# Kernel optimization log

Hardware: AMD Instinct MI355X
Metric: run time of the kernel (lower is better)

The kernel has to match this reference:

```python
import jax, jax.numpy as jnp
import numpy as np

N_NODES = 50000


def setup_inputs() -> dict:
    key = jax.random.key(0)
    ks = jax.random.split(key, 6)
    L, d = 3, 128
    x = jax.random.normal(ks[0], (N_NODES, d), dtype=jnp.float32)
    edge_index = jax.random.randint(ks[1], (2, 640000), 0, N_NODES, dtype=jnp.int64)
    s = 1.0 / np.sqrt(d)
    W1 = jax.random.normal(ks[2], (L, d, d), dtype=jnp.float32) * s
    W2 = jax.random.normal(ks[3], (L, d, d), dtype=jnp.float32) * s
    b1 = jnp.zeros((L, d), dtype=jnp.float32)
    b2 = jnp.zeros((L, d), dtype=jnp.float32)
    eps = jnp.zeros((L,), dtype=jnp.float32)
    final_w = jax.random.normal(ks[4], (d + L * d, d), dtype=jnp.float32) / np.sqrt(d + L * d)
    final_b = jnp.zeros((d,), dtype=jnp.float32)
    return {"x": x, "edge_index": edge_index, "W1": W1, "b1": b1,
            "W2": W2, "b2": b2, "eps": eps, "final_w": final_w, "final_b": final_b}


def reference(x, edge_index, W1, b1, W2, b2, eps, final_w, final_b):
    src, dst = edge_index[0], edge_index[1]
    num_layers = W1.shape[0]
    xs = [x]
    h = x
    for l in range(num_layers):
        # GINConv: sum-aggregate neighbor features, add (1+eps)*self, then 2-layer MLP
        agg = jax.ops.segment_sum(h[src], dst, num_segments=N_NODES)  # [N, d]
        z = (1.0 + eps[l]) * h + agg
        z = jax.nn.relu(z @ W1[l] + b1[l])
        h = jax.nn.relu(z @ W2[l] + b2[l])
        xs.append(h)
    out = jnp.concatenate(xs, axis=-1)  # [N, in + L*out]
    return out @ final_w + final_b
```

## Files before the change

### kernel.cpp

```cpp
#include <hip/hip_runtime.h>

#define NNODES 50000
#define NEDGES 640000
#define D 128

typedef unsigned short u16;
typedef unsigned int u32;
typedef __bf16 bf16x8 __attribute__((ext_vector_type(8)));
typedef float f32x4 __attribute__((ext_vector_type(4)));
union AB { uint4 u4; bf16x8 f; };

__device__ __forceinline__ u16 f2b(float f) {
    u32 u = __float_as_uint(f);
    return (u16)((u + 0x7fffu + ((u >> 16) & 1u)) >> 16);
}
__device__ __forceinline__ u32 pack2(float lo, float hi) {
    return (u32)f2b(lo) | ((u32)f2b(hi) << 16);
}
__device__ __forceinline__ float blo(u32 v) { return __uint_as_float(v << 16); }
__device__ __forceinline__ float bhi(u32 v) { return __uint_as_float(v & 0xffff0000u); }


__global__ void k_hist(const int* __restrict__ dst, int* __restrict__ cnt) {
    int e = blockIdx.x * 256 + threadIdx.x;
    if (e < NEDGES) atomicAdd(&cnt[dst[e]], 1);
}

__global__ void k_scan1(const int* __restrict__ cnt, int* __restrict__ rp,
                        int* __restrict__ bsum) {
    __shared__ int s[256];
    int tid = threadIdx.x;
    int i = blockIdx.x * 256 + tid;
    int v = (i < NNODES) ? cnt[i] : 0;
    s[tid] = v;
    __syncthreads();
    for (int off = 1; off < 256; off <<= 1) {
        int t = (tid >= off) ? s[tid - off] : 0;
        __syncthreads();
        s[tid] += t;
        __syncthreads();
    }
    if (i < NNODES) rp[i] = s[tid] - v;
    if (tid == 255) bsum[blockIdx.x] = s[255];
}

__global__ void k_scan2(int* __restrict__ bsum, int nb) {
    __shared__ int s[256];
    int tid = threadIdx.x;
    int v = (tid < nb) ? bsum[tid] : 0;
    s[tid] = v;
    __syncthreads();
    for (int off = 1; off < 256; off <<= 1) {
        int t = (tid >= off) ? s[tid - off] : 0;
        __syncthreads();
        s[tid] += t;
        __syncthreads();
    }
    if (tid < nb) bsum[tid] = s[tid] - v;
}

__global__ void k_add(int* __restrict__ rp, const int* __restrict__ bsum) {
    int i = blockIdx.x * 256 + threadIdx.x;
    if (i < NNODES) rp[i] += bsum[blockIdx.x];
    if (i == 0) rp[NNODES] = NEDGES;
}

__global__ void k_scatter(const int* __restrict__ src, const int* __restrict__ dst,
                          const int* __restrict__ rp, int* __restrict__ fill,
                          int* __restrict__ srcs) {
    int e = blockIdx.x * 256 + threadIdx.x;
    if (e < NEDGES) {
        int dn = dst[e];
        int p = rp[dn] + atomicAdd(&fill[dn], 1);
        srcs[p] = src[e];
    }
}

__global__ void k_prep(const float* __restrict__ W1, const float* __restrict__ W2,
                       const float* __restrict__ fw, u16* __restrict__ wT1,
                       u16* __restrict__ wT2, u16* __restrict__ fwTc) {
    int idx = blockIdx.x * 256 + threadIdx.x;
    if (idx < 3 * 16384) {
        int l = idx >> 14, r = idx & 16383, n = r >> 7, k = r & 127;
        wT1[idx] = f2b(W1[l * 16384 + k * 128 + n]);
        wT2[idx] = f2b(W2[l * 16384 + k * 128 + n]);
    }
    if (idx < 4 * 16384) {
        int ch = idx >> 14, r = idx & 16383, n = r >> 7, k = r & 127;
        fwTc[idx] = f2b(fw[(ch * 128 + k) * 128 + n]);
    }
}

__global__ void k_cvt(const float* __restrict__ x, u32* __restrict__ xb) {
    int i = blockIdx.x * 256 + threadIdx.x;
    if (i < NNODES * 64) {
        float2 v = ((const float2*)x)[i];
        xb[i] = pack2(v.x, v.y);
    }
}

__global__ void k_agg(const uint4* __restrict__ h4, const int* __restrict__ rp,
                      const int* __restrict__ srcs, const float* __restrict__ epsp,
                      uint4* __restrict__ z4) {
    int tid = threadIdx.x;
    int c = tid & 15;
    int node = (blockIdx.x * 256 + tid) >> 4;
    int gbase = tid & 48;
    float sc = 1.0f + epsp[0];

    uint4 sv = h4[node * 16 + c];
    float acc[8];
    acc[0] = sc * blo(sv.x); acc[1] = sc * bhi(sv.x);
    acc[2] = sc * blo(sv.y); acc[3] = sc * bhi(sv.y);
    acc[4] = sc * blo(sv.z); acc[5] = sc * bhi(sv.z);
    acc[6] = sc * blo(sv.w); acc[7] = sc * bhi(sv.w);

    int beg = rp[node], end = rp[node + 1];
    for (int base = beg; base < end; base += 16) {
        int n = end - base; if (n > 16) n = 16;
        int myidx = (base + c < end) ? srcs[base + c] : 0;
        int j = 0;
        for (; j + 4 <= n; j += 4) {
            int s0 = __shfl(myidx, gbase + j + 0, 64);
            int s1 = __shfl(myidx, gbase + j + 1, 64);
            int s2 = __shfl(myidx, gbase + j + 2, 64);
            int s3 = __shfl(myidx, gbase + j + 3, 64);
            uint4 v0 = h4[s0 * 16 + c];
            uint4 v1 = h4[s1 * 16 + c];
            uint4 v2 = h4[s2 * 16 + c];
            uint4 v3 = h4[s3 * 16 + c];
            acc[0] += blo(v0.x) + blo(v1.x) + blo(v2.x) + blo(v3.x);
            acc[1] += bhi(v0.x) + bhi(v1.x) + bhi(v2.x) + bhi(v3.x);
            acc[2] += blo(v0.y) + blo(v1.y) + blo(v2.y) + blo(v3.y);
            acc[3] += bhi(v0.y) + bhi(v1.y) + bhi(v2.y) + bhi(v3.y);
            acc[4] += blo(v0.z) + blo(v1.z) + blo(v2.z) + blo(v3.z);
            acc[5] += bhi(v0.z) + bhi(v1.z) + bhi(v2.z) + bhi(v3.z);
            acc[6] += blo(v0.w) + blo(v1.w) + blo(v2.w) + blo(v3.w);
            acc[7] += bhi(v0.w) + bhi(v1.w) + bhi(v2.w) + bhi(v3.w);
        }
        for (; j < n; ++j) {
            int s0 = __shfl(myidx, gbase + j, 64);
            uint4 v0 = h4[s0 * 16 + c];
            acc[0] += blo(v0.x); acc[1] += bhi(v0.x);
            acc[2] += blo(v0.y); acc[3] += bhi(v0.y);
            acc[4] += blo(v0.z); acc[5] += bhi(v0.z);
            acc[6] += blo(v0.w); acc[7] += bhi(v0.w);
        }
    }

    uint4 o;
    o.x = pack2(acc[0], acc[1]);
    o.y = pack2(acc[2], acc[3]);
    o.z = pack2(acc[4], acc[5]);
    o.w = pack2(acc[6], acc[7]);
    z4[node * 16 + c] = o;
}

__launch_bounds__(256, 2)
__global__ void k_mlp(const u16* __restrict__ A, const u16* __restrict__ wT1g,
                      const float* __restrict__ b1, const u16* __restrict__ wT2g,
                      const float* __restrict__ b2, u16* __restrict__ H) {
    __shared__ u16 wbuf[128 * 128];
    __shared__ u16 Tb[128 * 128];
    int tid = threadIdx.x;
    int wave = tid >> 6, lane = tid & 63, l16 = lane & 15, quad = lane >> 4;
    int r0 = blockIdx.x * 128 + wave * 32;

    {
        const uint4* g = (const uint4*)wT1g;
        for (int i = tid; i < 2048; i += 256) ((uint4*)wbuf)[i] = g[i];
    }

    AB a[2][4];
#pragma unroll
    for (int s = 0; s < 2; ++s) {
        int row = r0 + s * 16 + l16;
#pragma unroll
        for (int kb = 0; kb < 4; ++kb) {
            if (row < NNODES)
                a[s][kb].u4 = *(const uint4*)&A[row * 128 + kb * 32 + quad * 8];
            else
                a[s][kb].u4 = make_uint4(0, 0, 0, 0);
        }
    }
    __syncthreads();

    f32x4 acc[2][8];
#pragma unroll
    for (int col = 0; col < 8; ++col) {
        float bv = b1[col * 16 + l16];
        acc[0][col] = (f32x4){bv, bv, bv, bv};
        acc[1][col] = (f32x4){bv, bv, bv, bv};
    }
#pragma unroll
    for (int col = 0; col < 8; ++col) {
#pragma unroll
        for (int kb = 0; kb < 4; ++kb) {
            AB b;
            b.u4 = *(const uint4*)&wbuf[(col * 16 + l16) * 128 + kb * 32 + quad * 8];
            acc[0][col] = __builtin_amdgcn_mfma_f32_16x16x32_bf16(a[0][kb].f, b.f, acc[0][col], 0, 0, 0);
            acc[1][col] = __builtin_amdgcn_mfma_f32_16x16x32_bf16(a[1][kb].f, b.f, acc[1][col], 0, 0, 0);
        }
    }

#pragma unroll
    for (int s = 0; s < 2; ++s)
#pragma unroll
        for (int col = 0; col < 8; ++col)
#pragma unroll
            for (int r = 0; r < 4; ++r) {
                float v = fmaxf(acc[s][col][r], 0.f);
                Tb[(wave * 32 + s * 16 + quad * 4 + r) * 128 + col * 16 + l16] = f2b(v);
            }
    __syncthreads();

    {
        const uint4* g = (const uint4*)wT2g;
        for (int i = tid; i < 2048; i += 256) ((uint4*)wbuf)[i] = g[i];
    }
    AB a2[2][4];
#pragma unroll
    for (int s = 0; s < 2; ++s)
#pragma unroll
        for (int kb = 0; kb < 4; ++kb)
            a2[s][kb].u4 = *(const uint4*)&Tb[(wave * 32 + s * 16 + l16) * 128 + kb * 32 + quad * 8];
    __syncthreads();

#pragma unroll
    for (int col = 0; col < 8; ++col) {
        float bv = b2[col * 16 + l16];
        acc[0][col] = (f32x4){bv, bv, bv, bv};
        acc[1][col] = (f32x4){bv, bv, bv, bv};
    }
#pragma unroll
    for (int col = 0; col < 8; ++col) {
#pragma unroll
        for (int kb = 0; kb < 4; ++kb) {
            AB b;
            b.u4 = *(const uint4*)&wbuf[(col * 16 + l16) * 128 + kb * 32 + quad * 8];
            acc[0][col] = __builtin_amdgcn_mfma_f32_16x16x32_bf16(a2[0][kb].f, b.f, acc[0][col], 0, 0, 0);
            acc[1][col] = __builtin_amdgcn_mfma_f32_16x16x32_bf16(a2[1][kb].f, b.f, acc[1][col], 0, 0, 0);
        }
    }
#pragma unroll
    for (int s = 0; s < 2; ++s)
#pragma unroll
        for (int col = 0; col < 8; ++col)
#pragma unroll
            for (int r = 0; r < 4; ++r) {
                float v = fmaxf(acc[s][col][r], 0.f);
                Tb[(wave * 32 + s * 16 + quad * 4 + r) * 128 + col * 16 + l16] = f2b(v);
            }
    __syncthreads();

    for (int i = tid; i < 2048; i += 256) {
        int r = i >> 4, cc = i & 15;
        int grow = blockIdx.x * 128 + r;
        if (grow < NNODES)
            *(uint4*)&H[grow * 128 + cc * 8] = *(const uint4*)&Tb[r * 128 + cc * 8];
    }
}

__launch_bounds__(256, 2)
__global__ void k_final(const u16* __restrict__ xb, const u16* __restrict__ h1,
                        const u16* __restrict__ h2b, const u16* __restrict__ h3,
                        const u16* __restrict__ fwTc, const float* __restrict__ fb,
                        float* __restrict__ out) {
    __shared__ u16 wbuf[128 * 128];
    int tid = threadIdx.x;
    int wave = tid >> 6, lane = tid & 63, l16 = lane & 15, quad = lane >> 4;
    int r0 = blockIdx.x * 128 + wave * 32;

    f32x4 acc[2][8];
#pragma unroll
    for (int col = 0; col < 8; ++col) {
        float bv = fb[col * 16 + l16];
        acc[0][col] = (f32x4){bv, bv, bv, bv};
        acc[1][col] = (f32x4){bv, bv, bv, bv};
    }

    const u16* chin[4] = {xb, h1, h2b, h3};
    for (int ch = 0; ch < 4; ++ch) {
        __syncthreads();
        {
            const uint4* g = (const uint4*)(fwTc + ch * 16384);
            for (int i = tid; i < 2048; i += 256) ((uint4*)wbuf)[i] = g[i];
        }
        const u16* cp = chin[ch];
        AB a[2][4];
#pragma unroll
        for (int s = 0; s < 2; ++s) {
            int row = r0 + s * 16 + l16;
#pragma unroll
            for (int kb = 0; kb < 4; ++kb) {
                if (row < NNODES)
                    a[s][kb].u4 = *(const uint4*)&cp[row * 128 + kb * 32 + quad * 8];
                else
                    a[s][kb].u4 = make_uint4(0, 0, 0, 0);
            }
        }
        __syncthreads();
#pragma unroll
        for (int col = 0; col < 8; ++col) {
#pragma unroll
            for (int kb = 0; kb < 4; ++kb) {
                AB b;
                b.u4 = *(const uint4*)&wbuf[(col * 16 + l16) * 128 + kb * 32 + quad * 8];
                acc[0][col] = __builtin_amdgcn_mfma_f32_16x16x32_bf16(a[0][kb].f, b.f, acc[0][col], 0, 0, 0);
                acc[1][col] = __builtin_amdgcn_mfma_f32_16x16x32_bf16(a[1][kb].f, b.f, acc[1][col], 0, 0, 0);
            }
        }
    }

#pragma unroll
    for (int s = 0; s < 2; ++s)
#pragma unroll
        for (int col = 0; col < 8; ++col)
#pragma unroll
            for (int r = 0; r < 4; ++r) {
                int row = r0 + s * 16 + quad * 4 + r;
                if (row < NNODES) out[row * 128 + col * 16 + l16] = acc[s][col][r];
            }
}

extern "C" void kernel_launch(void* const* d_in, const int* in_sizes, int n_in,
                              void* d_out, int out_size, void* d_ws, size_t ws_size,
                              hipStream_t stream) {
    const float* x   = (const float*)d_in[0];
    const int*   ei  = (const int*)d_in[1];
    const float* W1  = (const float*)d_in[2];
    const float* b1  = (const float*)d_in[3];
    const float* W2  = (const float*)d_in[4];
    const float* b2  = (const float*)d_in[5];
    const float* eps = (const float*)d_in[6];
    const float* fw  = (const float*)d_in[7];
    const float* fb  = (const float*)d_in[8];
    float* out = (float*)d_out;

    const int* srcA = ei;
    const int* dstA = ei + NEDGES;

    char* p = (char*)d_ws;
    size_t off = 0;
    auto take = [&](size_t bytes) {
        char* r = p + off;
        off = (off + bytes + 255) & ~(size_t)255;
        return r;
    };
    int* rp   = (int*)take((NNODES + 1) * sizeof(int));
    int* cnt  = (int*)take(NNODES * sizeof(int));
    int* fill = (int*)take(NNODES * sizeof(int));
    int* bsum = (int*)take(256 * sizeof(int));
    int* srcs = (int*)take(NEDGES * sizeof(int));
    u16* wT1  = (u16*)take(3 * 16384 * sizeof(u16));
    u16* wT2  = (u16*)take(3 * 16384 * sizeof(u16));
    u16* fwTc = (u16*)take(4 * 16384 * sizeof(u16));
    u16* xb   = (u16*)take((size_t)NNODES * D * sizeof(u16));
    u16* zb   = (u16*)take((size_t)NNODES * D * sizeof(u16));
    u16* hb1  = (u16*)take((size_t)NNODES * D * sizeof(u16));
    u16* hb2  = (u16*)take((size_t)NNODES * D * sizeof(u16));
    u16* hb3  = (u16*)take((size_t)NNODES * D * sizeof(u16));
    (void)ws_size; (void)in_sizes; (void)n_in; (void)out_size;

    hipMemsetAsync(cnt, 0, NNODES * sizeof(int), stream);
    hipMemsetAsync(fill, 0, NNODES * sizeof(int), stream);

    k_prep<<<(4 * 16384 + 255) / 256, 256, 0, stream>>>(W1, W2, fw, wT1, wT2, fwTc);
    k_cvt<<<(NNODES * 64 + 255) / 256, 256, 0, stream>>>(x, (u32*)xb);

    int nb = (NNODES + 255) / 256;
    k_hist<<<(NEDGES + 255) / 256, 256, 0, stream>>>(dstA, cnt);
    k_scan1<<<nb, 256, 0, stream>>>(cnt, rp, bsum);
    k_scan2<<<1, 256, 0, stream>>>(bsum, nb);
    k_add<<<nb, 256, 0, stream>>>(rp, bsum);
    k_scatter<<<(NEDGES + 255) / 256, 256, 0, stream>>>(srcA, dstA, rp, fill, srcs);

    const u16* hin = xb;
    u16* houts[3] = {hb1, hb2, hb3};
    int gm = (NNODES + 127) / 128;
    for (int l = 0; l < 3; ++l) {
        k_agg<<<NNODES * 16 / 256, 256, 0, stream>>>((const uint4*)hin, rp, srcs, eps + l, (uint4*)zb);
        k_mlp<<<gm, 256, 0, stream>>>(zb, wT1 + l * 16384, b1 + l * D,
                                      wT2 + l * 16384, b2 + l * D, houts[l]);
        hin = houts[l];
    }
    k_final<<<gm, 256, 0, stream>>>(xb, hb1, hb2, hb3, fwTc, fb, out);
}
```

Measured before the change: 319.9 us.

## Fuse neighbor aggregation into MLP kernel with swizzled LDS and merged prep

Aggregation is now done inside the MLP kernel. Each block gathers and sums neighbor features for its 128 rows straight into shared memory, so the intermediate z buffer is no longer written to and read back from global memory, and three kernel launches are removed. Shared-memory tiles for weights and activations use an XOR-style chunk rotation to avoid bank conflicts, and the gather loop is unrolled to 8. The CSR scatter reuses the count array with atomicSub, which drops one memset, and the weight prep and x conversion are merged into one kernel. The risk is less parallelism in the gather: 391 blocks each walking 128 nodes serially, versus many small blocks before, which may leave memory latency less hidden.

```diff
diff --git a/kernel.cpp b/kernel.cpp
--- a/kernel.cpp
+++ b/kernel.cpp
@@ -19,6 +19,13 @@
 }
 __device__ __forceinline__ float blo(u32 v) { return __uint_as_float(v << 16); }
 __device__ __forceinline__ float bhi(u32 v) { return __uint_as_float(v & 0xffff0000u); }
+
+__device__ __forceinline__ void acc8(float* a, uint4 v) {
+    a[0] += blo(v.x); a[1] += bhi(v.x);
+    a[2] += blo(v.y); a[3] += bhi(v.y);
+    a[4] += blo(v.z); a[5] += bhi(v.z);
+    a[6] += blo(v.w); a[7] += bhi(v.w);
+}
 
 
 __global__ void k_hist(const int* __restrict__ dst, int* __restrict__ cnt) {
@@ -66,19 +73,20 @@
 }
 
 __global__ void k_scatter(const int* __restrict__ src, const int* __restrict__ dst,
-                          const int* __restrict__ rp, int* __restrict__ fill,
+                          const int* __restrict__ rp, int* __restrict__ cnt,
                           int* __restrict__ srcs) {
     int e = blockIdx.x * 256 + threadIdx.x;
     if (e < NEDGES) {
         int dn = dst[e];
-        int p = rp[dn] + atomicAdd(&fill[dn], 1);
-        srcs[p] = src[e];
+        int old = atomicSub(&cnt[dn], 1);
+        srcs[rp[dn] + old - 1] = src[e];
     }
 }
 
 __global__ void k_prep(const float* __restrict__ W1, const float* __restrict__ W2,
-                       const float* __restrict__ fw, u16* __restrict__ wT1,
-                       u16* __restrict__ wT2, u16* __restrict__ fwTc) {
+                       const float* __restrict__ fw, const float* __restrict__ x,
+                       u16* __restrict__ wT1, u16* __restrict__ wT2,
+                       u16* __restrict__ fwTc, u32* __restrict__ xb) {
     int idx = blockIdx.x * 256 + threadIdx.x;
     if (idx < 3 * 16384) {
         int l = idx >> 14, r = idx & 16383, n = r >> 7, k = r & 127;
@@ -89,101 +97,103 @@
         int ch = idx >> 14, r = idx & 16383, n = r >> 7, k = r & 127;
         fwTc[idx] = f2b(fw[(ch * 128 + k) * 128 + n]);
     }
-}
-
-__global__ void k_cvt(const float* __restrict__ x, u32* __restrict__ xb) {
-    int i = blockIdx.x * 256 + threadIdx.x;
-    if (i < NNODES * 64) {
-        float2 v = ((const float2*)x)[i];
-        xb[i] = pack2(v.x, v.y);
-    }
-}
-
-__global__ void k_agg(const uint4* __restrict__ h4, const int* __restrict__ rp,
+    if (idx < NNODES * 64) {
+        float2 v = ((const float2*)x)[idx];
+        xb[idx] = pack2(v.x, v.y);
+    }
+}
+
+__launch_bounds__(256, 2)
+__global__ void k_mlp(const uint4* __restrict__ h4, const int* __restrict__ rp,
                       const int* __restrict__ srcs, const float* __restrict__ epsp,
-                      uint4* __restrict__ z4) {
+                      const u16* __restrict__ wT1g, const float* __restrict__ b1,
+                      const u16* __restrict__ wT2g, const float* __restrict__ b2,
+                      u16* __restrict__ H) {
+    __shared__ u16 Tb[128 * 128];
+    __shared__ u16 wbuf[128 * 128];
+    uint4* Tb4 = (uint4*)Tb;
+    uint4* wb4 = (uint4*)wbuf;
     int tid = threadIdx.x;
-    int c = tid & 15;
-    int node = (blockIdx.x * 256 + tid) >> 4;
-    int gbase = tid & 48;
-    float sc = 1.0f + epsp[0];
-
-    uint4 sv = h4[node * 16 + c];
-    float acc[8];
-    acc[0] = sc * blo(sv.x); acc[1] = sc * bhi(sv.x);
-    acc[2] = sc * blo(sv.y); acc[3] = sc * bhi(sv.y);
-    acc[4] = sc * blo(sv.z); acc[5] = sc * bhi(sv.z);
-    acc[6] = sc * blo(sv.w); acc[7] = sc * bhi(sv.w);
-
-    int beg = rp[node], end = rp[node + 1];
-    for (int base = beg; base < end; base += 16) {
-        int n = end - base; if (n > 16) n = 16;
-        int myidx = (base + c < end) ? srcs[base + c] : 0;
-        int j = 0;
-        for (; j + 4 <= n; j += 4) {
-            int s0 = __shfl(myidx, gbase + j + 0, 64);
-            int s1 = __shfl(myidx, gbase + j + 1, 64);
-            int s2 = __shfl(myidx, gbase + j + 2, 64);
-            int s3 = __shfl(myidx, gbase + j + 3, 64);
-            uint4 v0 = h4[s0 * 16 + c];
-            uint4 v1 = h4[s1 * 16 + c];
-            uint4 v2 = h4[s2 * 16 + c];
-            uint4 v3 = h4[s3 * 16 + c];
-            acc[0] += blo(v0.x) + blo(v1.x) + blo(v2.x) + blo(v3.x);
-            acc[1] += bhi(v0.x) + bhi(v1.x) + bhi(v2.x) + bhi(v3.x);
-            acc[2] += blo(v0.y) + blo(v1.y) + blo(v2.y) + blo(v3.y);
-            acc[3] += bhi(v0.y) + bhi(v1.y) + bhi(v2.y) + bhi(v3.y);
-            acc[4] += blo(v0.z) + blo(v1.z) + blo(v2.z) + blo(v3.z);
-            acc[5] += bhi(v0.z) + bhi(v1.z) + bhi(v2.z) + bhi(v3.z);
-            acc[6] += blo(v0.w) + blo(v1.w) + blo(v2.w) + blo(v3.w);
-            acc[7] += bhi(v0.w) + bhi(v1.w) + bhi(v2.w) + bhi(v3.w);
-        }
-        for (; j < n; ++j) {
-            int s0 = __shfl(myidx, gbase + j, 64);
-            uint4 v0 = h4[s0 * 16 + c];
-            acc[0] += blo(v0.x); acc[1] += bhi(v0.x);
-            acc[2] += blo(v0.y); acc[3] += bhi(v0.y);
-            acc[4] += blo(v0.z); acc[5] += bhi(v0.z);
-            acc[6] += blo(v0.w); acc[7] += bhi(v0.w);
-        }
-    }
-
-    uint4 o;
-    o.x = pack2(acc[0], acc[1]);
-    o.y = pack2(acc[2], acc[3]);
-    o.z = pack2(acc[4], acc[5]);
-    o.w = pack2(acc[6], acc[7]);
-    z4[node * 16 + c] = o;
-}
-
-__launch_bounds__(256, 2)
-__global__ void k_mlp(const u16* __restrict__ A, const u16* __restrict__ wT1g,
-                      const float* __restrict__ b1, const u16* __restrict__ wT2g,
-                      const float* __restrict__ b2, u16* __restrict__ H) {
-    __shared__ u16 wbuf[128 * 128];
-    __shared__ u16 Tb[128 * 128];
-    int tid = threadIdx.x;
-    int wave = tid >> 6, lane = tid & 63, l16 = lane & 15, quad = lane >> 4;
-    int r0 = blockIdx.x * 128 + wave * 32;
+    int r0 = blockIdx.x * 128;
 
     {
         const uint4* g = (const uint4*)wT1g;
-        for (int i = tid; i < 2048; i += 256) ((uint4*)wbuf)[i] = g[i];
-    }
+        for (int i = tid; i < 2048; i += 256) {
+            int n = i >> 4, ch = i & 15;
+            wb4[n * 16 + ((ch + n) & 15)] = g[i];
+        }
+    }
+
+    {
+        int c = tid & 15;
+        int g16 = tid >> 4;
+        int gbase = tid & 48;
+        float sc = 1.0f + epsp[0];
+        for (int jn = 0; jn < 8; ++jn) {
+            int nl = g16 * 8 + jn;
+            int node = r0 + nl;
+            float acc[8] = {0.f, 0.f, 0.f, 0.f, 0.f, 0.f, 0.f, 0.f};
+            if (node < NNODES) {
+                uint4 sv = h4[node * 16 + c];
+                acc[0] = sc * blo(sv.x); acc[1] = sc * bhi(sv.x);
+                acc[2] = sc * blo(sv.y); acc[3] = sc * bhi(sv.y);
+                acc[4] = sc * blo(sv.z); acc[5] = sc * bhi(sv.z);
+                acc[6] = sc * blo(sv.w); acc[7] = sc * bhi(sv.w);
+                int beg = rp[node], end = rp[node + 1];
+                for (int base = beg; base < end; base += 16) {
+                    int n = end - base; if (n > 16) n = 16;
+                    int myidx = (base + c < end) ? srcs[base + c] : 0;
+                    int j = 0;
+                    for (; j + 8 <= n; j += 8) {
+                        int s0 = __shfl(myidx, gbase + j + 0, 64);
+                        int s1 = __shfl(myidx, gbase + j + 1, 64);
+                        int s2 = __shfl(myidx, gbase + j + 2, 64);
+                        int s3 = __shfl(myidx, gbase + j + 3, 64);
+                        int s4 = __shfl(myidx, gbase + j + 4, 64);
+                        int s5 = __shfl(myidx, gbase + j + 5, 64);
+                        int s6 = __shfl(myidx, gbase + j + 6, 64);
+                        int s7 = __shfl(myidx, gbase + j + 7, 64);
+                        uint4 v0 = h4[s0 * 16 + c]; uint4 v1 = h4[s1 * 16 + c];
+                        uint4 v2 = h4[s2 * 16 + c]; uint4 v3 = h4[s3 * 16 + c];
+                        uint4 v4 = h4[s4 * 16 + c]; uint4 v5 = h4[s5 * 16 + c];
+                        uint4 v6 = h4[s6 * 16 + c]; uint4 v7 = h4[s7 * 16 + c];
+                        acc8(acc, v0); acc8(acc, v1); acc8(acc, v2); acc8(acc, v3);
+                        acc8(acc, v4); acc8(acc, v5); acc8(acc, v6); acc8(acc, v7);
+                    }
+                    for (; j + 4 <= n; j += 4) {
+                        int s0 = __shfl(myidx, gbase + j + 0, 64);
+                        int s1 = __shfl(myidx, gbase + j + 1, 64);
+                        int s2 = __shfl(myidx, gbase + j + 2, 64);
+                        int s3 = __shfl(myidx, gbase + j + 3, 64);
+                        uint4 v0 = h4[s0 * 16 + c]; uint4 v1 = h4[s1 * 16 + c];
+                        uint4 v2 = h4[s2 * 16 + c]; uint4 v3 = h4[s3 * 16 + c];
+                        acc8(acc, v0); acc8(acc, v1); acc8(acc, v2); acc8(acc, v3);
+                    }
+                    for (; j < n; ++j) {
+                        int s0 = __shfl(myidx, gbase + j, 64);
+                        uint4 v0 = h4[s0 * 16 + c];
+                        acc8(acc, v0);
+                    }
+                }
+            }
+            uint4 o;
+            o.x = pack2(acc[0], acc[1]); o.y = pack2(acc[2], acc[3]);
+            o.z = pack2(acc[4], acc[5]); o.w = pack2(acc[6], acc[7]);
+            Tb4[nl * 16 + ((c + nl) & 15)] = o;
+        }
+    }
+    __syncthreads();
+
+    int wave = tid >> 6, lane = tid & 63, l16 = lane & 15, quad = lane >> 4;
 
     AB a[2][4];
 #pragma unroll
     for (int s = 0; s < 2; ++s) {
-        int row = r0 + s * 16 + l16;
-#pragma unroll
-        for (int kb = 0; kb < 4; ++kb) {
-            if (row < NNODES)
-                a[s][kb].u4 = *(const uint4*)&A[row * 128 + kb * 32 + quad * 8];
-            else
-                a[s][kb].u4 = make_uint4(0, 0, 0, 0);
-        }
-    }
-    __syncthreads();
+        int m = wave * 32 + s * 16 + l16;
+#pragma unroll
+        for (int kb = 0; kb < 4; ++kb)
+            a[s][kb].u4 = Tb4[m * 16 + ((kb * 4 + quad + m) & 15)];
+    }
 
     f32x4 acc[2][8];
 #pragma unroll
@@ -197,11 +207,13 @@
 #pragma unroll
         for (int kb = 0; kb < 4; ++kb) {
             AB b;
-            b.u4 = *(const uint4*)&wbuf[(col * 16 + l16) * 128 + kb * 32 + quad * 8];
+            int n = col * 16 + l16;
+            b.u4 = wb4[n * 16 + ((kb * 4 + quad + n) & 15)];
             acc[0][col] = __builtin_amdgcn_mfma_f32_16x16x32_bf16(a[0][kb].f, b.f, acc[0][col], 0, 0, 0);
             acc[1][col] = __builtin_amdgcn_mfma_f32_16x16x32_bf16(a[1][kb].f, b.f, acc[1][col], 0, 0, 0);
         }
     }
+    __syncthreads();
 
 #pragma unroll
     for (int s = 0; s < 2; ++s)
@@ -209,21 +221,29 @@
         for (int col = 0; col < 8; ++col)
 #pragma unroll
             for (int r = 0; r < 4; ++r) {
-                float v = fmaxf(acc[s][col][r], 0.f);
-                Tb[(wave * 32 + s * 16 + quad * 4 + r) * 128 + col * 16 + l16] = f2b(v);
+                int row = wave * 32 + s * 16 + quad * 4 + r;
+                int kcol = col * 16 + l16;
+                int ch = kcol >> 3;
+                Tb[row * 128 + ((ch + row) & 15) * 8 + (kcol & 7)] =
+                    f2b(fmaxf(acc[s][col][r], 0.f));
             }
     __syncthreads();
 
     {
         const uint4* g = (const uint4*)wT2g;
-        for (int i = tid; i < 2048; i += 256) ((uint4*)wbuf)[i] = g[i];
+        for (int i = tid; i < 2048; i += 256) {
+            int n = i >> 4, ch = i & 15;
+            wb4[n * 16 + ((ch + n) & 15)] = g[i];
+        }
     }
     AB a2[2][4];
 #pragma unroll
-    for (int s = 0; s < 2; ++s)
+    for (int s = 0; s < 2; ++s) {
+        int m = wave * 32 + s * 16 + l16;
 #pragma unroll
         for (int kb = 0; kb < 4; ++kb)
-            a2[s][kb].u4 = *(const uint4*)&Tb[(wave * 32 + s * 16 + l16) * 128 + kb * 32 + quad * 8];
+            a2[s][kb].u4 = Tb4[m * 16 + ((kb * 4 + quad + m) & 15)];
+    }
     __syncthreads();
 
 #pragma unroll
@@ -237,27 +257,33 @@
 #pragma unroll
         for (int kb = 0; kb < 4; ++kb) {
             AB b;
-            b.u4 = *(const uint4*)&wbuf[(col * 16 + l16) * 128 + kb * 32 + quad * 8];
+            int n = col * 16 + l16;
+            b.u4 = wb4[n * 16 + ((kb * 4 + quad + n) & 15)];
             acc[0][col] = __builtin_amdgcn_mfma_f32_16x16x32_bf16(a2[0][kb].f, b.f, acc[0][col], 0, 0, 0);
             acc[1][col] = __builtin_amdgcn_mfma_f32_16x16x32_bf16(a2[1][kb].f, b.f, acc[1][col], 0, 0, 0);
         }
     }
+    __syncthreads();
+
 #pragma unroll
     for (int s = 0; s < 2; ++s)
 #pragma unroll
         for (int col = 0; col < 8; ++col)
 #pragma unroll
             for (int r = 0; r < 4; ++r) {
-                float v = fmaxf(acc[s][col][r], 0.f);
-                Tb[(wave * 32 + s * 16 + quad * 4 + r) * 128 + col * 16 + l16] = f2b(v);
+                int row = wave * 32 + s * 16 + quad * 4 + r;
+                int kcol = col * 16 + l16;
+                int ch = kcol >> 3;
+                Tb[row * 128 + ((ch + row) & 15) * 8 + (kcol & 7)] =
+                    f2b(fmaxf(acc[s][col][r], 0.f));
             }
     __syncthreads();
 
     for (int i = tid; i < 2048; i += 256) {
-        int r = i >> 4, cc = i & 15;
-        int grow = blockIdx.x * 128 + r;
+        int r = i >> 4, ch = i & 15;
+        int grow = r0 + r;
         if (grow < NNODES)
-            *(uint4*)&H[grow * 128 + cc * 8] = *(const uint4*)&Tb[r * 128 + cc * 8];
+            *(uint4*)&H[grow * 128 + ch * 8] = Tb4[r * 16 + ((ch + r) & 15)];
     }
 }
 
@@ -267,6 +293,7 @@
                         const u16* __restrict__ fwTc, const float* __restrict__ fb,
                         float* __restrict__ out) {
     __shared__ u16 wbuf[128 * 128];
+    uint4* wb4 = (uint4*)wbuf;
     int tid = threadIdx.x;
     int wave = tid >> 6, lane = tid & 63, l16 = lane & 15, quad = lane >> 4;
     int r0 = blockIdx.x * 128 + wave * 32;
@@ -280,13 +307,16 @@
     }
 
     const u16* chin[4] = {xb, h1, h2b, h3};
-    for (int ch = 0; ch < 4; ++ch) {
+    for (int chn = 0; chn < 4; ++chn) {
         __syncthreads();
         {
-            const uint4* g = (const uint4*)(fwTc + ch * 16384);
-            for (int i = tid; i < 2048; i += 256) ((uint4*)wbuf)[i] = g[i];
-        }
-        const u16* cp = chin[ch];
+            const uint4* g = (const uint4*)(fwTc + chn * 16384);
+            for (int i = tid; i < 2048; i += 256) {
+                int n = i >> 4, ch = i & 15;
+                wb4[n * 16 + ((ch + n) & 15)] = g[i];
+            }
+        }
+        const u16* cp = chin[chn];
         AB a[2][4];
 #pragma unroll
         for (int s = 0; s < 2; ++s) {
@@ -305,7 +335,8 @@
 #pragma unroll
             for (int kb = 0; kb < 4; ++kb) {
                 AB b;
-                b.u4 = *(const uint4*)&wbuf[(col * 16 + l16) * 128 + kb * 32 + quad * 8];
+                int n = col * 16 + l16;
+                b.u4 = wb4[n * 16 + ((kb * 4 + quad + n) & 15)];
                 acc[0][col] = __builtin_amdgcn_mfma_f32_16x16x32_bf16(a[0][kb].f, b.f, acc[0][col], 0, 0, 0);
                 acc[1][col] = __builtin_amdgcn_mfma_f32_16x16x32_bf16(a[1][kb].f, b.f, acc[1][col], 0, 0, 0);
             }
@@ -349,38 +380,33 @@
     };
     int* rp   = (int*)take((NNODES + 1) * sizeof(int));
     int* cnt  = (int*)take(NNODES * sizeof(int));
-    int* fill = (int*)take(NNODES * sizeof(int));
     int* bsum = (int*)take(256 * sizeof(int));
     int* srcs = (int*)take(NEDGES * sizeof(int));
     u16* wT1  = (u16*)take(3 * 16384 * sizeof(u16));
     u16* wT2  = (u16*)take(3 * 16384 * sizeof(u16));
     u16* fwTc = (u16*)take(4 * 16384 * sizeof(u16));
     u16* xb   = (u16*)take((size_t)NNODES * D * sizeof(u16));
-    u16* zb   = (u16*)take((size_t)NNODES * D * sizeof(u16));
     u16* hb1  = (u16*)take((size_t)NNODES * D * sizeof(u16));
     u16* hb2  = (u16*)take((size_t)NNODES * D * sizeof(u16));
     u16* hb3  = (u16*)take((size_t)NNODES * D * sizeof(u16));
     (void)ws_size; (void)in_sizes; (void)n_in; (void)out_size;
 
     hipMemsetAsync(cnt, 0, NNODES * sizeof(int), stream);
-    hipMemsetAsync(fill, 0, NNODES * sizeof(int), stream);
-
-    k_prep<<<(4 * 16384 + 255) / 256, 256, 0, stream>>>(W1, W2, fw, wT1, wT2, fwTc);
-    k_cvt<<<(NNODES * 64 + 255) / 256, 256, 0, stream>>>(x, (u32*)xb);
 
     int nb = (NNODES + 255) / 256;
     k_hist<<<(NEDGES + 255) / 256, 256, 0, stream>>>(dstA, cnt);
     k_scan1<<<nb, 256, 0, stream>>>(cnt, rp, bsum);
     k_scan2<<<1, 256, 0, stream>>>(bsum, nb);
     k_add<<<nb, 256, 0, stream>>>(rp, bsum);
-    k_scatter<<<(NEDGES + 255) / 256, 256, 0, stream>>>(srcA, dstA, rp, fill, srcs);
+    k_scatter<<<(NEDGES + 255) / 256, 256, 0, stream>>>(srcA, dstA, rp, cnt, srcs);
+    k_prep<<<(NNODES * 64 + 255) / 256, 256, 0, stream>>>(W1, W2, fw, x, wT1, wT2, fwTc, (u32*)xb);
 
     const u16* hin = xb;
     u16* houts[3] = {hb1, hb2, hb3};
     int gm = (NNODES + 127) / 128;
     for (int l = 0; l < 3; ++l) {
-        k_agg<<<NNODES * 16 / 256, 256, 0, stream>>>((const uint4*)hin, rp, srcs, eps + l, (uint4*)zb);
-        k_mlp<<<gm, 256, 0, stream>>>(zb, wT1 + l * 16384, b1 + l * D,
+        k_mlp<<<gm, 256, 0, stream>>>((const uint4*)hin, rp, srcs, eps + l,
+                                      wT1 + l * 16384, b1 + l * D,
                                       wT2 + l * 16384, b2 + l * D, houts[l]);
         hin = houts[l];
     }
```

New measurement: 332.1 us. 3.8% more time.
